# Optimization experiments

Hardware: AMD Instinct MI355X
Metric: run time of the kernel (lower is better)

Reference implementation:

```python
import jax, jax.numpy as jnp
import numpy as np

B, E, H, SEQ = 4096, 512, 512, 128


def setup_inputs() -> dict:
    key = jax.random.key(0)
    ks = jax.random.split(key, 7)
    s = 1.0 / np.sqrt(H)  # PyTorch LSTM init scale
    return {
        "start_emb": jax.random.normal(ks[0], (B, 1, E), dtype=jnp.float32),
        "h0": jax.random.normal(ks[1], (1, B, H), dtype=jnp.float32),
        "c0": jax.random.normal(ks[2], (1, B, H), dtype=jnp.float32),
        "w_ih": jax.random.normal(ks[3], (4 * H, E), dtype=jnp.float32) * s,
        "w_hh": jax.random.normal(ks[4], (4 * H, H), dtype=jnp.float32) * s,
        "b_ih": jax.random.normal(ks[5], (4 * H,), dtype=jnp.float32) * s,
        "b_hh": jax.random.normal(ks[6], (4 * H,), dtype=jnp.float32) * s,
        "seq_length": SEQ,
    }


def reference(start_emb, h0, c0, w_ih, w_hh, b_ih, b_hh, seq_length):
    # start_emb: [B, 1, E] -- identical input every step, so precompute its projection once.
    x = start_emb[:, 0, :]                       # [B, E]
    x_proj = x @ w_ih.T + b_ih + b_hh            # [B, 4H], constant across steps
    hdim = w_hh.shape[1]

    def step(carry, _):
        h, c = carry                              # each [B, H]
        gates = x_proj + h @ w_hh.T               # [B, 4H]
        i, f, g, o = jnp.split(gates, 4, axis=-1) # PyTorch gate order i,f,g,o
        i = jax.nn.sigmoid(i)
        f = jax.nn.sigmoid(f)
        g = jnp.tanh(g)
        o = jax.nn.sigmoid(o)
        c = f * c + i * g
        h = o * jnp.tanh(c)
        return (h, c), None

    (h, c), _ = jax.lax.scan(step, (h0[0], c0[0]), None, length=seq_length)
    # Return final (h_n, c_n) with the [num_layers=1, B, H] leading dim, as PyTorch does.
    return h[None], c[None]
```

## Files before the change

kernel.cpp:

```cpp
#include <hip/hip_runtime.h>
#include <hip/hip_bf16.h>

#define BATCH 4096
#define KD    512
#define NG    2048
#define SEQLEN 128

typedef __attribute__((ext_vector_type(8))) short short8;
typedef __attribute__((ext_vector_type(4))) float floatx4;

#define HWREG_XCC_ID (20 | (0 << 6) | ((4 - 1) << 11))

__device__ __forceinline__ void gld16(const void* g, void* l) {
  __builtin_amdgcn_global_load_lds(
      (const __attribute__((address_space(1))) void*)g,
      (__attribute__((address_space(3))) void*)l, 16, 0, 0);
}

__device__ __forceinline__ float fast_sig(float x) {
  return __builtin_amdgcn_rcpf(1.0f + __expf(-x));
}
__device__ __forceinline__ float fast_tanh(float x) {
  return 1.0f - 2.0f * __builtin_amdgcn_rcpf(1.0f + __expf(2.0f * x));
}

__device__ __forceinline__ unsigned pack_bf16(float lo, float hi) {
  unsigned ul = (unsigned)__builtin_bit_cast(unsigned short, __float2bfloat16(lo));
  unsigned uh = (unsigned)__builtin_bit_cast(unsigned short, __float2bfloat16(hi));
  return (uh << 16) | ul;
}
__device__ __forceinline__ float unpack_lo(unsigned u) {
  u <<= 16; return __builtin_bit_cast(float, u);
}
__device__ __forceinline__ float unpack_hi(unsigned u) {
  u &= 0xffff0000u; return __builtin_bit_cast(float, u);
}

__device__ __forceinline__ void load_panel128(const short* __restrict__ W, int bn,
                                              short* __restrict__ lWB, int tid) {
#pragma unroll
  for (int i = 0; i < 16; ++i) {
    int q = i * 512 + tid;
    int kt = q >> 10;
    int rem = q & 1023;
    int row = rem >> 3, cc = rem & 7;
    int cs = cc ^ (row & 7);
    gld16(W + (size_t)(bn + row) * KD + (kt * 8 + cs) * 8, lWB + q * 8);
  }
}

__device__ __forceinline__ void gemm_panel(const short* __restrict__ A,
                                           const short* __restrict__ lWB,
                                           short* __restrict__ lA,
                                           floatx4 acc[4][4],
                                           int bm, int lane, int wm, int wn,
                                           int tid) {
#pragma unroll 1
  for (int kt = 0; kt < 8; ++kt) {
    const int k0 = kt * 64;
#pragma unroll
    for (int i = 0; i < 4; ++i) {
      int q = i * 512 + tid;
      int row = q >> 3, cs = q & 7;
      int cc = cs ^ (row & 7);
      gld16(A + (size_t)(bm + row) * KD + k0 + cc * 8, lA + q * 8);
    }
    __syncthreads();
#pragma unroll
    for (int ks = 0; ks < 2; ++ks) {
      short8 a[4], b[4];
#pragma unroll
      for (int mi = 0; mi < 4; ++mi) {
        int arow = wm * 64 + mi * 16 + (lane & 15);
        int ch = (ks * 4 + (lane >> 4)) ^ (arow & 7);
        a[mi] = *(const short8*)&lA[arow * 64 + ch * 8];
      }
#pragma unroll
      for (int j = 0; j < 4; ++j) {
        int brow = wn * 64 + j * 16 + (lane & 15);
        int cc = (ks * 4 + (lane >> 4)) ^ (brow & 7);
        b[j] = *(const short8*)&lWB[kt * 8192 + brow * 64 + cc * 8];
      }
#pragma unroll
      for (int mi = 0; mi < 4; ++mi)
#pragma unroll
        for (int j = 0; j < 4; ++j)
          acc[mi][j] =
              __builtin_amdgcn_mfma_f32_16x16x32_bf16(a[mi], b[j], acc[mi][j], 0, 0, 0);
    }
    __syncthreads();
  }
}

template <int TBM, int TBN, int NT>
__device__ __forceinline__ void gemm_tile(const short* __restrict__ A,
                                          const short* __restrict__ Bw,
                                          floatx4 acc[4][4],
                                          short* lA, short* lB,
                                          int bm, int bn,
                                          int lane, int wm, int wn, int tid) {
#pragma unroll 1
  for (int kt = 0; kt < KD / 64; ++kt) {
    const int k0 = kt * 64;
#pragma unroll
    for (int i = 0; i < TBM * 8 / NT; ++i) {
      int q = i * NT + tid;
      int row = q >> 3, cs = q & 7;
      int cc = cs ^ (row & 7);
      gld16(A + (size_t)(bm + row) * KD + k0 + cc * 8, lA + q * 8);
    }
#pragma unroll
    for (int i = 0; i < TBN * 8 / NT; ++i) {
      int q = i * NT + tid;
      int row = q >> 3, cs = q & 7;
      int cc = cs ^ (row & 7);
      gld16(Bw + (size_t)(bn + row) * KD + k0 + cc * 8, lB + q * 8);
    }
    __syncthreads();
#pragma unroll
    for (int ks = 0; ks < 2; ++ks) {
      short8 a[4], b[4];
#pragma unroll
      for (int mi = 0; mi < 4; ++mi) {
        int arow = wm * 64 + mi * 16 + (lane & 15);
        int ch = (ks * 4 + (lane >> 4)) ^ (arow & 7);
        a[mi] = *(const short8*)&lA[arow * 64 + ch * 8];
      }
#pragma unroll
      for (int j = 0; j < 4; ++j) {
        int brow = wn * 64 + j * 16 + (lane & 15);
        int ch = (ks * 4 + (lane >> 4)) ^ (brow & 7);
        b[j] = *(const short8*)&lB[brow * 64 + ch * 8];
      }
#pragma unroll
      for (int mi = 0; mi < 4; ++mi)
#pragma unroll
        for (int j = 0; j < 4; ++j)
          acc[mi][j] =
              __builtin_amdgcn_mfma_f32_16x16x32_bf16(a[mi], b[j], acc[mi][j], 0, 0, 0);
    }
    __syncthreads();
  }
}

__device__ __forceinline__ void group_barrier_xcd(unsigned* cnt, unsigned target) {
  __syncthreads();
  if (threadIdx.x == 0) {
    __hip_atomic_fetch_add(cnt, 1u, __ATOMIC_RELAXED, __HIP_MEMORY_SCOPE_AGENT);
    unsigned guard = 0;
    while (__hip_atomic_load(cnt, __ATOMIC_RELAXED, __HIP_MEMORY_SCOPE_AGENT) <
               target &&
           ++guard < (1u << 20)) {
      __builtin_amdgcn_s_sleep(1);
    }
    asm volatile("buffer_inv sc0" ::: "memory");
    asm volatile("s_waitcnt vmcnt(0)" ::: "memory");
  }
  __syncthreads();
}

__global__ __launch_bounds__(512, 1) void lstm_persist(
    const short* __restrict__ xbf,
    const short* __restrict__ wih,
    const short* __restrict__ whh,
    const float* __restrict__ biasp,
    const float* __restrict__ c0,
    short* __restrict__ hA, short* __restrict__ hB,
    float* __restrict__ outH, float* __restrict__ outC,
    unsigned* __restrict__ sync_area) {
  extern __shared__ __align__(16) char dsm[];
  short* lWB = (short*)dsm;
  short* lA  = (short*)(dsm + 131072);

  const int tid = threadIdx.x;
  const int lane = tid & 63;
  const int wid = tid >> 6;
  const int wm = wid >> 1;
  const int wn = wid & 1;

  if (tid == 0) {
    int px = __builtin_amdgcn_s_getreg(HWREG_XCC_ID) & 7;
    unsigned r = __hip_atomic_fetch_add(&sync_area[px], 1u, __ATOMIC_RELAXED,
                                        __HIP_MEMORY_SCOPE_AGENT);
    ((int*)lA)[0] = px * 2 + (int)((r >> 4) & 1);
    ((int*)lA)[1] = (int)(r & 15);
  }
  __syncthreads();
  const int gid = ((int*)lA)[0];
  const int by  = ((int*)lA)[1];
  __syncthreads();
  const int bm = gid * 256;
  const int bn = by * 128;
  unsigned* gcnt = sync_area + 256 + gid * 32;

  const int houter = by * 2 + wn;
  const int hcol = houter * 16 + (lane & 15);
  const int rb = houter * 64 + (lane & 15);

  load_panel128(wih, bn, lWB, tid);
  __syncthreads();
  floatx4 acc[4][4] = {};
  gemm_panel(xbf, lWB, lA, acc, bm, lane, wm, wn, tid);

  const float b0 = biasp[rb], b1 = biasp[rb + 16], b2 = biasp[rb + 32],
              b3 = biasp[rb + 48];
  unsigned xprP[4][4][2];
  float creg[4][4];
#pragma unroll
  for (int mi = 0; mi < 4; ++mi) {
    const int mrow0 = bm + wm * 64 + mi * 16 + (lane >> 4) * 4;
#pragma unroll
    for (int reg = 0; reg < 4; ++reg) {
      xprP[mi][reg][0] = pack_bf16(acc[mi][0][reg] + b0, acc[mi][1][reg] + b1);
      xprP[mi][reg][1] = pack_bf16(acc[mi][2][reg] + b2, acc[mi][3][reg] + b3);
      creg[mi][reg] = c0[(size_t)(mrow0 + reg) * KD + hcol];
    }
  }

  load_panel128(whh, bn, lWB, tid);
  __syncthreads();

#pragma unroll 1
  for (int t = 0; t < SEQLEN; ++t) {
    const short* hin = (t & 1) ? hB : hA;
    short* hout = (t & 1) ? hA : hB;

#pragma unroll
    for (int mi = 0; mi < 4; ++mi)
#pragma unroll
      for (int j = 0; j < 4; ++j)
        acc[mi][j] = floatx4{0.f, 0.f, 0.f, 0.f};

    gemm_panel(hin, lWB, lA, acc, bm, lane, wm, wn, tid);

#pragma unroll
    for (int mi = 0; mi < 4; ++mi) {
      const int mrow0 = bm + wm * 64 + mi * 16 + (lane >> 4) * 4;
#pragma unroll
      for (int reg = 0; reg < 4; ++reg) {
        const int m = mrow0 + reg;
        float gi = acc[mi][0][reg] + unpack_lo(xprP[mi][reg][0]);
        float gf = acc[mi][1][reg] + unpack_hi(xprP[mi][reg][0]);
        float gg = acc[mi][2][reg] + unpack_lo(xprP[mi][reg][1]);
        float go = acc[mi][3][reg] + unpack_hi(xprP[mi][reg][1]);
        float si = fast_sig(gi);
        float sf = fast_sig(gf);
        float tg = fast_tanh(gg);
        float so = fast_sig(go);
        float cn = sf * creg[mi][reg] + si * tg;
        creg[mi][reg] = cn;
        float hn = so * fast_tanh(cn);
        const size_t ci = (size_t)m * KD + hcol;
        ((__hip_bfloat16*)hout)[ci] = __float2bfloat16(hn);
        if (t == SEQLEN - 1) {
          outH[ci] = hn;
          outC[ci] = cn;
        }
      }
    }
    if (t != SEQLEN - 1) group_barrier_xcd(gcnt, 16u * (unsigned)(t + 1));
  }
}

__global__ __launch_bounds__(256, 2) void lstm_step(
    const short* __restrict__ hin, __hip_bfloat16* __restrict__ hout_bf,
    const short* __restrict__ W, const float* __restrict__ xp,
    float* __restrict__ c, float* __restrict__ hout_f32) {
  __shared__ __align__(16) short lA[128 * 64];
  __shared__ __align__(16) short lB[128 * 64];
  const int tid = threadIdx.x;
  const int lane = tid & 63;
  const int wid = tid >> 6;
  const int wm = wid >> 1, wn = wid & 1;
  const int bm = blockIdx.x * 128, bn = blockIdx.y * 128;

  floatx4 acc[4][4] = {};
  gemm_tile<128, 128, 256>(hin, W, acc, lA, lB, bm, bn, lane, wm, wn, tid);

  const int houter = blockIdx.y * 2 + wn;
  const int hcol = houter * 16 + (lane & 15);
  const int rb = houter * 64 + (lane & 15);
#pragma unroll
  for (int mi = 0; mi < 4; ++mi) {
    const int mrow0 = bm + wm * 64 + mi * 16 + (lane >> 4) * 4;
#pragma unroll
    for (int reg = 0; reg < 4; ++reg) {
      const int m = mrow0 + reg;
      const float* xpr = xp + (size_t)m * NG + rb;
      float si = fast_sig(acc[mi][0][reg] + xpr[0]);
      float sf = fast_sig(acc[mi][1][reg] + xpr[16]);
      float tg = fast_tanh(acc[mi][2][reg] + xpr[32]);
      float so = fast_sig(acc[mi][3][reg] + xpr[48]);
      const int ci = m * KD + hcol;
      float cn = sf * c[ci] + si * tg;
      c[ci] = cn;
      float hn = so * fast_tanh(cn);
      hout_bf[ci] = __float2bfloat16(hn);
      if (hout_f32) hout_f32[ci] = hn;
    }
  }
}

__global__ __launch_bounds__(256, 2) void xproj_gemm(
    const short* __restrict__ xbf, const short* __restrict__ Wih,
    const float* __restrict__ biasp, float* __restrict__ xp) {
  __shared__ __align__(16) short lA[128 * 64];
  __shared__ __align__(16) short lB[128 * 64];
  const int tid = threadIdx.x;
  const int lane = tid & 63;
  const int wid = tid >> 6;
  const int wm = wid >> 1, wn = wid & 1;
  const int bm = blockIdx.x * 128, bn = blockIdx.y * 128;

  floatx4 acc[4][4] = {};
  gemm_tile<128, 128, 256>(xbf, Wih, acc, lA, lB, bm, bn, lane, wm, wn, tid);

  const int houter = blockIdx.y * 2 + wn;
  const int rb = houter * 64 + (lane & 15);
  const float b0 = biasp[rb], b1 = biasp[rb + 16], b2 = biasp[rb + 32],
              b3 = biasp[rb + 48];
#pragma unroll
  for (int mi = 0; mi < 4; ++mi) {
    const int mrow0 = bm + wm * 64 + mi * 16 + (lane >> 4) * 4;
#pragma unroll
    for (int reg = 0; reg < 4; ++reg) {
      float* xpr = xp + (size_t)(mrow0 + reg) * NG + rb;
      xpr[0]  = acc[mi][0][reg] + b0;
      xpr[16] = acc[mi][1][reg] + b1;
      xpr[32] = acc[mi][2][reg] + b2;
      xpr[48] = acc[mi][3][reg] + b3;
    }
  }
}

__global__ void permw_k(const float* __restrict__ w,
                        __hip_bfloat16* __restrict__ o) {
  int idx = blockIdx.x * 256 + threadIdx.x;
  int r = idx >> 9, k = idx & 511;
  int hout = r >> 6, g = (r >> 4) & 3, hin = r & 15;
  o[idx] = __float2bfloat16(w[(size_t)((g << 9) + hout * 16 + hin) * 512 + k]);
}

__global__ void bias_k(const float* __restrict__ bi, const float* __restrict__ bh,
                       float* __restrict__ o) {
  int r = blockIdx.x * 256 + threadIdx.x;
  int hout = r >> 6, g = (r >> 4) & 3, hin = r & 15;
  int n = (g << 9) + hout * 16 + hin;
  o[r] = bi[n] + bh[n];
}

__global__ void f2bf_k(const float* __restrict__ in,
                       __hip_bfloat16* __restrict__ out, int n) {
  int i = blockIdx.x * 256 + threadIdx.x;
  if (i < n) out[i] = __float2bfloat16(in[i]);
}

extern "C" void kernel_launch(void* const* d_in, const int* in_sizes, int n_in,
                              void* d_out, int out_size, void* d_ws, size_t ws_size,
                              hipStream_t stream) {
  const float* start_emb = (const float*)d_in[0];
  const float* h0 = (const float*)d_in[1];
  const float* c0 = (const float*)d_in[2];
  const float* w_ih = (const float*)d_in[3];
  const float* w_hh = (const float*)d_in[4];
  const float* b_ih = (const float*)d_in[5];
  const float* b_hh = (const float*)d_in[6];

  char* ws = (char*)d_ws;
  __hip_bfloat16* whh_p = (__hip_bfloat16*)(ws);
  __hip_bfloat16* wih_p = (__hip_bfloat16*)(ws + (2ll << 20));
  __hip_bfloat16* xbf   = (__hip_bfloat16*)(ws + (4ll << 20));
  __hip_bfloat16* hbufA = (__hip_bfloat16*)(ws + (8ll << 20));
  __hip_bfloat16* hbufB = (__hip_bfloat16*)(ws + (12ll << 20));
  float* biasp          = (float*)(ws + (16ll << 20));
  unsigned* sync_area   = (unsigned*)(ws + (16ll << 20) + 65536);
  float* xp             = (float*)(ws + (17ll << 20));

  float* outH = (float*)d_out;
  float* outC = (float*)d_out + (size_t)BATCH * KD;

  permw_k<<<4096, 256, 0, stream>>>(w_hh, whh_p);
  permw_k<<<4096, 256, 0, stream>>>(w_ih, wih_p);
  bias_k<<<8, 256, 0, stream>>>(b_ih, b_hh, biasp);
  f2bf_k<<<8192, 256, 0, stream>>>(start_emb, xbf, BATCH * KD);
  f2bf_k<<<8192, 256, 0, stream>>>(h0, hbufA, BATCH * KD);
  (void)hipMemsetAsync(sync_area, 0, 8192, stream);

  const short* a_xbf = (const short*)xbf;
  const short* a_wih = (const short*)wih_p;
  const short* a_whh = (const short*)whh_p;
  const float* a_bias = biasp;
  const float* a_c0 = c0;
  short* a_hA = (short*)hbufA;
  short* a_hB = (short*)hbufB;
  float* a_outH = outH;
  float* a_outC = outC;
  unsigned* a_sync = sync_area;
  void* args[] = {&a_xbf, &a_wih, &a_whh, &a_bias, &a_c0,
                  &a_hA, &a_hB, &a_outH, &a_outC, &a_sync};
  hipError_t e = hipLaunchCooperativeKernel((const void*)lstm_persist,
                                            dim3(256), dim3(512), args,
                                            163840, stream);
  if (e != hipSuccess) {
    (void)hipMemcpyAsync(outC, c0, (size_t)BATCH * KD * sizeof(float),
                         hipMemcpyDeviceToDevice, stream);
    dim3 grid(BATCH / 128, NG / 128);
    xproj_gemm<<<grid, 256, 0, stream>>>((const short*)xbf, (const short*)wih_p,
                                         biasp, xp);
    for (int t = 0; t < SEQLEN; ++t) {
      const short* hin = (const short*)((t & 1) ? hbufB : hbufA);
      __hip_bfloat16* hout = (t & 1) ? hbufA : hbufB;
      lstm_step<<<grid, 256, 0, stream>>>(hin, hout, (const short*)whh_p, xp,
                                          outC, (t == SEQLEN - 1) ? outH : nullptr);
    }
  }
}
```

Measured before the change: 1.535 ms.

## Double-buffer A-tile staging in the persistent LSTM GEMM with 32-wide k-steps

Replaces the single-buffered 64-wide k-tile loop with a double-buffered 32-wide pipeline. The next h/x slice is prefetched into LDS via global_load_lds while MFMAs consume the current one, and there is one barrier per step instead of two. The goal is to hide global-load latency of the recurrent state inside the per-timestep GEMM. In exchange it doubles the number of loop iterations and barriers per k-range, and uses a new swizzled two-rows-per-LDS-row layout for A.

```diff
diff --git a/kernel.cpp b/kernel.cpp
--- a/kernel.cpp
+++ b/kernel.cpp
@@ -49,45 +49,60 @@
   }
 }
 
-__device__ __forceinline__ void gemm_panel(const short* __restrict__ A,
-                                           const short* __restrict__ lWB,
-                                           short* __restrict__ lA,
-                                           floatx4 acc[4][4],
-                                           int bm, int lane, int wm, int wn,
-                                           int tid) {
-#pragma unroll 1
-  for (int kt = 0; kt < 8; ++kt) {
-    const int k0 = kt * 64;
-#pragma unroll
-    for (int i = 0; i < 4; ++i) {
-      int q = i * 512 + tid;
-      int row = q >> 3, cs = q & 7;
-      int cc = cs ^ (row & 7);
-      gld16(A + (size_t)(bm + row) * KD + k0 + cc * 8, lA + q * 8);
-    }
-    __syncthreads();
-#pragma unroll
-    for (int ks = 0; ks < 2; ++ks) {
-      short8 a[4], b[4];
-#pragma unroll
-      for (int mi = 0; mi < 4; ++mi) {
-        int arow = wm * 64 + mi * 16 + (lane & 15);
-        int ch = (ks * 4 + (lane >> 4)) ^ (arow & 7);
-        a[mi] = *(const short8*)&lA[arow * 64 + ch * 8];
-      }
-#pragma unroll
-      for (int j = 0; j < 4; ++j) {
-        int brow = wn * 64 + j * 16 + (lane & 15);
-        int cc = (ks * 4 + (lane >> 4)) ^ (brow & 7);
-        b[j] = *(const short8*)&lWB[kt * 8192 + brow * 64 + cc * 8];
-      }
-#pragma unroll
-      for (int mi = 0; mi < 4; ++mi)
-#pragma unroll
-        for (int j = 0; j < 4; ++j)
-          acc[mi][j] =
-              __builtin_amdgcn_mfma_f32_16x16x32_bf16(a[mi], b[j], acc[mi][j], 0, 0, 0);
-    }
+__device__ __forceinline__ void stageA32(const short* __restrict__ A, int bm,
+                                         int p, short* __restrict__ dst, int tid) {
+  const int k0 = p * 32;
+#pragma unroll
+  for (int i = 0; i < 2; ++i) {
+    int q = i * 512 + tid;
+    int lr = q >> 3, c1 = q & 7;
+    int c0 = c1 ^ (lr & 7);
+    int row = lr * 2 + (c0 >> 2);
+    int kc = c0 & 3;
+    gld16(A + (size_t)(bm + row) * KD + k0 + kc * 8, dst + q * 8);
+  }
+}
+
+__device__ __forceinline__ void compute32(const short* __restrict__ lWB,
+                                          const short* __restrict__ lA,
+                                          floatx4 acc[4][4], int p,
+                                          int lane, int wm, int wn) {
+  short8 a[4], b[4];
+  const int kt = p >> 1;
+  const int kb = (p & 1) * 4 + (lane >> 4);
+#pragma unroll
+  for (int j = 0; j < 4; ++j) {
+    int brow = wn * 64 + j * 16 + (lane & 15);
+    int cc = kb ^ (brow & 7);
+    b[j] = *(const short8*)&lWB[kt * 8192 + brow * 64 + cc * 8];
+  }
+#pragma unroll
+  for (int mi = 0; mi < 4; ++mi) {
+    int arow = wm * 64 + mi * 16 + (lane & 15);
+    int lr = arow >> 1;
+    int cc = (((arow & 1) << 2) + (lane >> 4)) ^ (lr & 7);
+    a[mi] = *(const short8*)&lA[lr * 64 + cc * 8];
+  }
+#pragma unroll
+  for (int mi = 0; mi < 4; ++mi)
+#pragma unroll
+    for (int j = 0; j < 4; ++j)
+      acc[mi][j] =
+          __builtin_amdgcn_mfma_f32_16x16x32_bf16(a[mi], b[j], acc[mi][j], 0, 0, 0);
+}
+
+__device__ __forceinline__ void gemm_dbuf(const short* __restrict__ A,
+                                          const short* __restrict__ lWB,
+                                          short* __restrict__ lAb,
+                                          floatx4 acc[4][4],
+                                          int bm, int lane, int wm, int wn,
+                                          int tid) {
+  stageA32(A, bm, 0, lAb, tid);
+  __syncthreads();
+#pragma unroll 2
+  for (int p = 0; p < 16; ++p) {
+    if (p < 15) stageA32(A, bm, p + 1, lAb + ((p + 1) & 1) * 8192, tid);
+    compute32(lWB, lAb + (p & 1) * 8192, acc, p, lane, wm, wn);
     __syncthreads();
   }
 }
@@ -170,7 +185,7 @@
     unsigned* __restrict__ sync_area) {
   extern __shared__ __align__(16) char dsm[];
   short* lWB = (short*)dsm;
-  short* lA  = (short*)(dsm + 131072);
+  short* lAb = (short*)(dsm + 131072);
 
   const int tid = threadIdx.x;
   const int lane = tid & 63;
@@ -182,12 +197,12 @@
     int px = __builtin_amdgcn_s_getreg(HWREG_XCC_ID) & 7;
     unsigned r = __hip_atomic_fetch_add(&sync_area[px], 1u, __ATOMIC_RELAXED,
                                         __HIP_MEMORY_SCOPE_AGENT);
-    ((int*)lA)[0] = px * 2 + (int)((r >> 4) & 1);
-    ((int*)lA)[1] = (int)(r & 15);
-  }
-  __syncthreads();
-  const int gid = ((int*)lA)[0];
-  const int by  = ((int*)lA)[1];
+    ((int*)lAb)[0] = px * 2 + (int)((r >> 4) & 1);
+    ((int*)lAb)[1] = (int)(r & 15);
+  }
+  __syncthreads();
+  const int gid = ((int*)lAb)[0];
+  const int by  = ((int*)lAb)[1];
   __syncthreads();
   const int bm = gid * 256;
   const int bn = by * 128;
@@ -200,7 +215,7 @@
   load_panel128(wih, bn, lWB, tid);
   __syncthreads();
   floatx4 acc[4][4] = {};
-  gemm_panel(xbf, lWB, lA, acc, bm, lane, wm, wn, tid);
+  gemm_dbuf(xbf, lWB, lAb, acc, bm, lane, wm, wn, tid);
 
   const float b0 = biasp[rb], b1 = biasp[rb + 16], b2 = biasp[rb + 32],
               b3 = biasp[rb + 48];
@@ -231,7 +246,7 @@
       for (int j = 0; j < 4; ++j)
         acc[mi][j] = floatx4{0.f, 0.f, 0.f, 0.f};
 
-    gemm_panel(hin, lWB, lA, acc, bm, lane, wm, wn, tid);
+    gemm_dbuf(hin, lWB, lAb, acc, bm, lane, wm, wn, tid);
 
 #pragma unroll
     for (int mi = 0; mi < 4; ++mi) {
```

After: 1.445 ms, median of 2. -5.8%, faster.
